# Kernel optimization log

Measured on AMD Instinct MI355X. Metric: run time of the kernel, lower is better.

## Reference

```python
import jax, jax.numpy as jnp
import numpy as np

EPS = 1e-5

def chan_layernorm(x, g):
    # LayerNorm over channel dim (-3), unbiased=False variance, learned scale g [C]
    mean = jnp.mean(x, axis=1, keepdims=True)
    var = jnp.var(x, axis=1, keepdims=True)
    return (x - mean) * jax.lax.rsqrt(var + EPS) * g[None, :, None, None]

def conv1x1(x, w):
    # w: [out_c, in_c]; pointwise conv == channel GEMM
    return jnp.einsum('bchw,oc->bohw', x, w)

def dwconv3x3(x, w):
    # depthwise 3x3, padding=1; w: [C, 1, 3, 3]
    C = x.shape[1]
    return jax.lax.conv_general_dilated(
        x, w, window_strides=(1, 1), padding='SAME',
        feature_group_count=C,
        dimension_numbers=('NCHW', 'OIHW', 'NCHW'))

def setup_inputs() -> dict:
    key = jax.random.key(0)
    ks = jax.random.split(key, 8)
    b, dim, x, y = 8, 512, 64, 64
    s1 = (dim ** -0.5) * 0.5  # modest init scale
    sd = (9 ** -0.5)
    return {
        'fmap': jax.random.normal(ks[0], (b, dim, x, y), jnp.float32),
        'g': jnp.ones((dim,), jnp.float32),
        'wq1': jax.random.normal(ks[1], (dim, dim), jnp.float32) * s1,
        'wq_dw': jax.random.normal(ks[2], (dim, 1, 3, 3), jnp.float32) * sd,
        'wk1': jax.random.normal(ks[3], (dim, dim), jnp.float32) * s1,
        'wk_dw': jax.random.normal(ks[4], (dim, 1, 3, 3), jnp.float32) * sd,
        'wv1': jax.random.normal(ks[5], (dim, dim), jnp.float32) * s1,
        'wv_dw': jax.random.normal(ks[6], (dim, 1, 3, 3), jnp.float32) * sd,
        'w_out': jax.random.normal(ks[7], (dim, dim), jnp.float32) * s1,
    }

def reference(fmap, g, wq1, wq_dw, wk1, wk_dw, wv1, wv_dw, w_out):
    b, dim, x, y = fmap.shape
    h = 8
    d = dim // h
    scale = d ** -0.5

    fm = chan_layernorm(fmap, g)
    q = dwconv3x3(conv1x1(fm, wq1), wq_dw)
    k = dwconv3x3(conv1x1(fm, wk1), wk_dw)
    v = dwconv3x3(conv1x1(fm, wv1), wv_dw)

    # b (h c) x y -> (b h) (x y) c
    def split_heads(t):
        return t.reshape(b, h, d, x * y).transpose(0, 1, 3, 2).reshape(b * h, x * y, d)
    q, k, v = map(split_heads, (q, k, v))

    q = jax.nn.softmax(q, axis=-1) * scale  # softmax over feature dim
    k = jax.nn.softmax(k, axis=-2)          # softmax over token dim

    ctx = jnp.einsum('bnd,bne->bde', k, v)  # [bh, d, d]
    out = jnp.einsum('bnd,bde->bne', q, ctx)  # [bh, n, d]

    # (b h) (x y) d -> b (h d) x y
    out = out.reshape(b, h, x * y, d).transpose(0, 1, 3, 2).reshape(b, h * d, x, y)
    out = jax.nn.silu(out)
    return conv1x1(out, w_out)
```

## Files before the change

### kernel.cpp

```cpp
#include <hip/hip_runtime.h>
#include <hip/hip_bf16.h>

typedef __attribute__((ext_vector_type(8))) short short8;
typedef __attribute__((ext_vector_type(4))) short shortx4;
typedef __attribute__((ext_vector_type(4))) float floatx4;

#define NB 8
#define C 512
#define NSP 4096
#define NHD 8
#define HDD 64

using bf16 = __hip_bfloat16;

__device__ __forceinline__ float b2f(bf16 v) { return __bfloat162float(v); }
__device__ __forceinline__ bf16 f2b(float f) { return __float2bfloat16(f); }
__device__ __forceinline__ float s2f(short s) {
    union { float f; unsigned u; } cv; cv.u = ((unsigned)(unsigned short)s) << 16; return cv.f;
}
__device__ __forceinline__ short f2s(float f) {
    bf16 b = f2b(f); return *reinterpret_cast<short*>(&b);
}

__device__ __forceinline__ void gl2lds16(const bf16* g, bf16* l) {
#if __has_builtin(__builtin_amdgcn_global_load_lds)
    __builtin_amdgcn_global_load_lds(
        (const __attribute__((address_space(1))) unsigned int*)g,
        (__attribute__((address_space(3))) unsigned int*)l, 16, 0, 0);
#else
    *(short8*)l = *(const short8*)g;
#endif
}

__global__ void detect_dtype(const unsigned* __restrict__ g_raw, int* __restrict__ flag) {
    *flag = (g_raw[0] == 0x3F800000u) ? 1 : 0;
}

__global__ __launch_bounds__(256) void prep_w(const void* g, const void* w1q, const void* wdq,
                                              const void* w1k, const void* wdk,
                                              const void* w1v, const void* wdv, const void* w1o,
                                              bf16* gc, bf16* wqkv, bf16* woutc,
                                              bf16* wkdc, bf16* wvdc, bf16* wqdT,
                                              const int* flag) {
    int i = blockIdx.x * 256 + threadIdx.x;
    int f = *flag;
    auto cv = [&](const void* s, int j) -> bf16 {
        return f ? f2b(((const float*)s)[j]) : ((const bf16*)s)[j];
    };
    if (i < C * C) {
        wqkv[i] = cv(w1q, i);
        wqkv[C * C + i] = cv(w1k, i);
        wqkv[2 * C * C + i] = cv(w1v, i);
        woutc[i] = cv(w1o, i);
    }
    if (i < C * 9) {
        int c = i / 9, t = i - c * 9;
        wqdT[t * C + c] = cv(wdq, i);
        wkdc[i] = cv(wdk, i);
        wvdc[i] = cv(wdv, i);
    }
    if (i < C) gc[i] = cv(g, i);
}

__global__ __launch_bounds__(256) void ln_fused(const void* __restrict__ fmap,
                                                const bf16* __restrict__ gc,
                                                bf16* __restrict__ fm,
                                                const int* __restrict__ flag) {
    const int P = 516;
    __shared__ bf16 T[32 * P];
    __shared__ float stat[32][2];
    int b = blockIdx.y;
    int n0 = blockIdx.x * 32;
    int t = threadIdx.x;
    if (*flag) {
        int nq = t & 7;
        int c0 = t >> 3;
        const float* src = (const float*)fmap + (size_t)b * C * NSP + n0 + nq * 4;
#pragma unroll 4
        for (int it = 0; it < 16; ++it) {
            int c = c0 + it * 32;
            float4 v = *(const float4*)(src + (size_t)c * NSP);
            T[(nq * 4 + 0) * P + c] = f2b(v.x);
            T[(nq * 4 + 1) * P + c] = f2b(v.y);
            T[(nq * 4 + 2) * P + c] = f2b(v.z);
            T[(nq * 4 + 3) * P + c] = f2b(v.w);
        }
    } else {
        int nq = t & 3;
        int c0 = t >> 2;
        const bf16* src = (const bf16*)fmap + (size_t)b * C * NSP + n0 + nq * 8;
#pragma unroll 4
        for (int it = 0; it < 8; ++it) {
            int c = c0 + it * 64;
            union { short8 s; short h[8]; } v;
            v.s = *(const short8*)(src + (size_t)c * NSP);
#pragma unroll
            for (int j = 0; j < 8; ++j)
                *(short*)&T[(nq * 8 + j) * P + c] = v.h[j];
        }
    }
    __syncthreads();
    int n = t >> 3, part = t & 7;
    {
        float s = 0.f, sq = 0.f;
        const bf16* row = T + n * P + part * 64;
#pragma unroll
        for (int i = 0; i < 8; ++i) {
            union { short8 v; short h[8]; } u;
            u.v = *(const short8*)(row + i * 8);
#pragma unroll
            for (int j = 0; j < 8; ++j) { float x = s2f(u.h[j]); s += x; sq += x * x; }
        }
#pragma unroll
        for (int off = 1; off < 8; off <<= 1) {
            s += __shfl_xor(s, off, 64);
            sq += __shfl_xor(sq, off, 64);
        }
        if (part == 0) {
            float mean = s * (1.f / C);
            float var = sq * (1.f / C) - mean * mean;
            stat[n][0] = mean;
            stat[n][1] = rsqrtf(var + 1e-5f);
        }
    }
    __syncthreads();
    float mean = stat[n][0], rs = stat[n][1];
    bf16* dst = fm + ((size_t)b * NSP + n0 + n) * C + part * 64;
    const bf16* row = T + n * P + part * 64;
    const bf16* gp = gc + part * 64;
#pragma unroll
    for (int i = 0; i < 8; ++i) {
        union { short8 v; short h[8]; } u, gv, ov;
        u.v = *(const short8*)(row + i * 8);
        gv.v = *(const short8*)(gp + i * 8);
#pragma unroll
        for (int j = 0; j < 8; ++j)
            ov.h[j] = f2s((s2f(u.h[j]) - mean) * rs * s2f(gv.h[j]));
        *(short8*)(dst + i * 8) = ov.v;
    }
}

template <int PHASE>
__global__ __launch_bounds__(512, 2) void gemm256(const bf16* __restrict__ X,
                                                  const bf16* __restrict__ Wall,
                                                  void* __restrict__ O0,
                                                  void* __restrict__ O1,
                                                  void* __restrict__ O2,
                                                  const int* __restrict__ flag) {
    __shared__ __align__(16) bf16 SH[4][256 * 64];
    bf16* SA0 = SH[0];
    bf16* SA1 = SH[1];
    bf16* SB0 = SH[2];
    bf16* SB1 = SH[3];
    const int nbase = blockIdx.x * 256;
    const int obase = blockIdx.y * 256;
    const int b = blockIdx.z;
    const int t = threadIdx.x;
    const int lane = t & 63, w = t >> 6;
    const int wm = w >> 2, wn = w & 3;
    const int m16 = lane & 15, q = lane >> 4;
    const bool AisW = (PHASE == 0) && (obase < 512);
    const bf16* gX = X + (size_t)b * NSP * C + (size_t)nbase * C;
    const bf16* gW = Wall + (size_t)obase * C;
    const bf16* gA = AisW ? gW : gX;
    const bf16* gB = AisW ? gX : gW;

    const int srow = t >> 3;
    const int sch = ((t & 7) ^ (srow & 7)) * 8;

    const int rA = wm * 128 + m16;
    const int rB = wn * 64 + m16;
    const int cs0 = ((q) ^ (m16 & 7)) * 8;
    const int cs1 = ((4 + q) ^ (m16 & 7)) * 8;

    floatx4 acc[8][4] = {};
    short8 Bf[4][2];

#define STAGE(LDS, G, K0, H)                                                   \
    {                                                                          \
        const bf16* _s = (G) + (size_t)((H) * 128 + srow) * C + (K0) + sch;    \
        bf16* _d = (LDS) + (H) * 8192 + t * 8;                                 \
        gl2lds16(_s, _d);                                                      \
        gl2lds16(_s + 64 * C, _d + 4096);                                      \
    }

#define VMW(N)                                                                 \
    {                                                                          \
        asm volatile("s_waitcnt vmcnt(" #N ")" ::: "memory");                  \
        __builtin_amdgcn_sched_barrier(0);                                     \
    }

#define PH(J, LA, LB, LOADB, STAGE_STMT, WAIT_STMT)                            \
    {                                                                          \
        short8 Af0, Af1, Af2, Af3;                                             \
        if (LOADB) {                                                           \
            _Pragma("unroll") for (int nt = 0; nt < 4; ++nt) {                 \
                Bf[nt][0] = *(const short8*)((LB) + (rB + nt * 16) * 64 + cs0);\
                Bf[nt][1] = *(const short8*)((LB) + (rB + nt * 16) * 64 + cs1);\
            }                                                                  \
        }                                                                      \
        Af0 = *(const short8*)((LA) + (rA + (2 * (J)) * 16) * 64 + cs0);       \
        Af1 = *(const short8*)((LA) + (rA + (2 * (J)) * 16) * 64 + cs1);       \
        Af2 = *(const short8*)((LA) + (rA + (2 * (J) + 1) * 16) * 64 + cs0);   \
        Af3 = *(const short8*)((LA) + (rA + (2 * (J) + 1) * 16) * 64 + cs1);   \
        STAGE_STMT;                                                            \
        WAIT_STMT;                                                             \
        __builtin_amdgcn_sched_barrier(0);                                     \
        __builtin_amdgcn_s_barrier();                                          \
        asm volatile("s_waitcnt lgkmcnt(0)" ::: "memory");                     \
        __builtin_amdgcn_sched_barrier(0);                                     \
        __builtin_amdgcn_s_setprio(1);                                         \
        _Pragma("unroll") for (int nt = 0; nt < 4; ++nt) {                     \
            acc[2 * (J)][nt] = __builtin_amdgcn_mfma_f32_16x16x32_bf16(        \
                Af0, Bf[nt][0], acc[2 * (J)][nt], 0, 0, 0);                    \
            acc[2 * (J)][nt] = __builtin_amdgcn_mfma_f32_16x16x32_bf16(        \
                Af1, Bf[nt][1], acc[2 * (J)][nt], 0, 0, 0);                    \
            acc[2 * (J) + 1][nt] = __builtin_amdgcn_mfma_f32_16x16x32_bf16(    \
                Af2, Bf[nt][0], acc[2 * (J) + 1][nt], 0, 0, 0);                \
            acc[2 * (J) + 1][nt] = __builtin_amdgcn_mfma_f32_16x16x32_bf16(    \
                Af3, Bf[nt][1], acc[2 * (J) + 1][nt], 0, 0, 0);                \
        }                                                                      \
        __builtin_amdgcn_s_setprio(0);                                         \
        __builtin_amdgcn_sched_barrier(0);                                     \
        __builtin_amdgcn_s_barrier();                                          \
    }

    STAGE(SA0, gA, 0, 0);
    STAGE(SA0, gA, 0, 1);
    STAGE(SB0, gB, 0, 0);
    STAGE(SB0, gB, 0, 1);
    STAGE(SB1, gB, 64, 0);
    STAGE(SB1, gB, 64, 1);
    VMW(0);
    __builtin_amdgcn_s_barrier();

    for (int i = 0; i < 3; ++i) {
        int kT = i * 128;
        PH(0, SA0, SB0, true,  STAGE(SA1, gA, kT + 64, 0),  ((void)0));
        PH(1, SA0, SB0, false, STAGE(SA1, gA, kT + 64, 1),  ((void)0));
        PH(2, SA0, SB0, false, STAGE(SB0, gB, kT + 128, 0), ((void)0));
        PH(3, SA0, SB0, false, STAGE(SB0, gB, kT + 128, 1), VMW(4));
        PH(0, SA1, SB1, true,  STAGE(SA0, gA, kT + 128, 0), ((void)0));
        PH(1, SA1, SB1, false, STAGE(SA0, gA, kT + 128, 1), ((void)0));
        PH(2, SA1, SB1, false, STAGE(SB1, gB, kT + 192, 0), ((void)0));
        PH(3, SA1, SB1, false, STAGE(SB1, gB, kT + 192, 1), VMW(4));
    }
    PH(0, SA0, SB0, true,  STAGE(SA1, gA, 448, 0), ((void)0));
    PH(1, SA0, SB0, false, STAGE(SA1, gA, 448, 1), ((void)0));
    PH(2, SA0, SB0, false, ((void)0), ((void)0));
    PH(3, SA0, SB0, false, ((void)0), VMW(0));
    PH(0, SA1, SB1, true,  ((void)0), ((void)0));
    PH(1, SA1, SB1, false, ((void)0), ((void)0));
    PH(2, SA1, SB1, false, ((void)0), ((void)0));
    PH(3, SA1, SB1, false, ((void)0), ((void)0));

#undef PH
#undef VMW
#undef STAGE

    if (PHASE == 0 && AisW) {
        bf16* out = (bf16*)O0 + (size_t)b * NSP * C;
#pragma unroll
        for (int nt = 0; nt < 4; ++nt)
#pragma unroll
            for (int mt = 0; mt < 8; ++mt) {
                int n = nbase + wn * 64 + nt * 16 + m16;
                int o = obase + wm * 128 + mt * 16 + q * 4;
                shortx4 pv;
#pragma unroll
                for (int r = 0; r < 4; ++r) pv[r] = f2s(acc[mt][nt][r]);
                *(shortx4*)(out + (size_t)n * C + o) = pv;
            }
    } else if (PHASE == 0) {
        bf16* out = (bf16*)((obase < 1024) ? O1 : O2) + (size_t)b * C * NSP;
        int ob = obase & 511;
#pragma unroll
        for (int nt = 0; nt < 4; ++nt)
#pragma unroll
            for (int mt = 0; mt < 8; ++mt) {
                int o = ob + wn * 64 + nt * 16 + m16;
                int n = nbase + wm * 128 + mt * 16 + q * 4;
                shortx4 pv;
#pragma unroll
                for (int r = 0; r < 4; ++r) pv[r] = f2s(acc[mt][nt][r]);
                *(shortx4*)(out + (size_t)o * NSP + n) = pv;
            }
    } else {
        int is_f32 = *flag;
        size_t outb = (size_t)b * C * NSP;
#pragma unroll
        for (int nt = 0; nt < 4; ++nt)
#pragma unroll
            for (int mt = 0; mt < 8; ++mt) {
                int o = obase + wn * 64 + nt * 16 + m16;
                int n = nbase + wm * 128 + mt * 16 + q * 4;
                size_t off = outb + (size_t)o * NSP + n;
                if (is_f32) {
                    *(floatx4*)((float*)O0 + off) = acc[mt][nt];
                } else {
                    shortx4 pv;
#pragma unroll
                    for (int r = 0; r < 4; ++r) pv[r] = f2s(acc[mt][nt][r]);
                    *(shortx4*)((bf16*)O0 + off) = pv;
                }
            }
    }
}

__global__ __launch_bounds__(256) void dwconv_nc8_sm(const bf16* __restrict__ X,
                                                     const bf16* __restrict__ WdT,
                                                     bf16* __restrict__ O) {
    int idx = blockIdx.x * 256 + threadIdx.x;
    int cg = idx & 63;
    int n = (idx >> 6) & (NSP - 1);
    int b = idx >> 18;
    int c0 = cg * 8;
    int y = n >> 6, x = n & 63;
    const bf16* xp = X + (size_t)b * NSP * C + c0;
    union { short8 s; short h[8]; } wv[9];
#pragma unroll
    for (int t = 0; t < 9; ++t) wv[t].s = *(const short8*)(WdT + t * C + c0);
    float acc[8] = {};
#pragma unroll
    for (int ky = 0; ky < 3; ++ky) {
        int yy = y + ky - 1;
        if ((unsigned)yy >= 64u) continue;
#pragma unroll
        for (int kx = 0; kx < 3; ++kx) {
            int xx = x + kx - 1;
            if ((unsigned)xx >= 64u) continue;
            union { short8 s; short h[8]; } iv;
            iv.s = *(const short8*)(xp + (size_t)(yy * 64 + xx) * C);
            int t = ky * 3 + kx;
#pragma unroll
            for (int i = 0; i < 8; ++i)
                acc[i] += s2f(iv.h[i]) * s2f(wv[t].h[i]);
        }
    }
    float mx = acc[0];
#pragma unroll
    for (int i = 1; i < 8; ++i) mx = fmaxf(mx, acc[i]);
#pragma unroll
    for (int off = 1; off < 8; off <<= 1) mx = fmaxf(mx, __shfl_xor(mx, off, 64));
    float e[8], s = 0.f;
#pragma unroll
    for (int i = 0; i < 8; ++i) { e[i] = __expf(acc[i] - mx); s += e[i]; }
#pragma unroll
    for (int off = 1; off < 8; off <<= 1) s += __shfl_xor(s, off, 64);
    float inv = 0.125f / s;
    union { short8 s; short h[8]; } ov;
#pragma unroll
    for (int i = 0; i < 8; ++i) ov.h[i] = f2s(e[i] * inv);
    *(short8*)(O + ((size_t)(b * NSP) + n) * C + c0) = ov.s;
}

__global__ __launch_bounds__(256) void dw_sk(const bf16* __restrict__ X,
                                             const bf16* __restrict__ Wd,
                                             bf16* __restrict__ O) {
    int bc = blockIdx.x;
    int c = bc & (C - 1);
    int t = threadIdx.x;
    int y = t >> 2, x0 = (t & 3) * 16;
    const bf16* xp = X + (size_t)bc * NSP;
    float wv[9];
#pragma unroll
    for (int i = 0; i < 9; ++i) wv[i] = b2f(Wd[c * 9 + i]);
    float a[16];
#pragma unroll
    for (int i = 0; i < 16; ++i) a[i] = 0.f;
#pragma unroll
    for (int ky = 0; ky < 3; ++ky) {
        int yy = y + ky - 1;
        if ((unsigned)yy >= 64u) continue;
        const bf16* rp = xp + yy * 64;
        float v[18];
        v[0] = (x0 > 0) ? b2f(rp[x0 - 1]) : 0.f;
        union { short8 s; short h[8]; } m0, m1;
        m0.s = *(const short8*)(rp + x0);
        m1.s = *(const short8*)(rp + x0 + 8);
#pragma unroll
        for (int j = 0; j < 8; ++j) { v[1 + j] = s2f(m0.h[j]); v[9 + j] = s2f(m1.h[j]); }
        v[17] = (x0 < 48) ? b2f(rp[x0 + 16]) : 0.f;
#pragma unroll
        for (int i = 0; i < 16; ++i)
            a[i] += wv[ky * 3 + 0] * v[i] + wv[ky * 3 + 1] * v[i + 1] + wv[ky * 3 + 2] * v[i + 2];
    }
    float mx = a[0];
#pragma unroll
    for (int i = 1; i < 16; ++i) mx = fmaxf(mx, a[i]);
#pragma unroll
    for (int off = 32; off; off >>= 1) mx = fmaxf(mx, __shfl_xor(mx, off, 64));
    __shared__ float red[4];
    __shared__ float bcv;
    int lane = t & 63, wid = t >> 6;
    if (lane == 0) red[wid] = mx;
    __syncthreads();
    if (t == 0) bcv = fmaxf(fmaxf(red[0], red[1]), fmaxf(red[2], red[3]));
    __syncthreads();
    float M = bcv;
    float s = 0.f;
#pragma unroll
    for (int i = 0; i < 16; ++i) { a[i] = __expf(a[i] - M); s += a[i]; }
#pragma unroll
    for (int off = 32; off; off >>= 1) s += __shfl_xor(s, off, 64);
    __syncthreads();
    if (lane == 0) red[wid] = s;
    __syncthreads();
    if (t == 0) bcv = red[0] + red[1] + red[2] + red[3];
    __syncthreads();
    float inv = 1.f / bcv;
    union { short8 s8; short h[8]; } o0, o1;
#pragma unroll
    for (int j = 0; j < 8; ++j) { o0.h[j] = f2s(a[j] * inv); o1.h[j] = f2s(a[8 + j] * inv); }
    bf16* op = O + (size_t)bc * NSP + y * 64 + x0;
    *(short8*)op = o0.s8;
    *(short8*)(op + 8) = o1.s8;
}

__global__ __launch_bounds__(256) void dwconv_cn8(const bf16* __restrict__ X,
                                                  const bf16* __restrict__ Wd,
                                                  bf16* __restrict__ O) {
    int idx = blockIdx.x * 256 + threadIdx.x;
    int g = idx & 511;
    int bc = idx >> 9;
    int c = bc & (C - 1);
    int y = g >> 3, x0 = (g & 7) * 8;
    const bf16* xp = X + (size_t)bc * NSP;
    float w[9];
#pragma unroll
    for (int t = 0; t < 9; ++t) w[t] = b2f(Wd[c * 9 + t]);
    float acc[8] = {};
#pragma unroll
    for (int ky = 0; ky < 3; ++ky) {
        int yy = y + ky - 1;
        if ((unsigned)yy >= 64u) continue;
        const bf16* rp = xp + yy * 64;
        union { short8 s; short h[8]; } mv;
        mv.s = *(const short8*)(rp + x0);
        float vals[10];
        vals[0] = (x0 > 0) ? b2f(rp[x0 - 1]) : 0.f;
#pragma unroll
        for (int i = 0; i < 8; ++i) vals[i + 1] = s2f(mv.h[i]);
        vals[9] = (x0 < 56) ? b2f(rp[x0 + 8]) : 0.f;
#pragma unroll
        for (int i = 0; i < 8; ++i)
            acc[i] += w[ky * 3 + 0] * vals[i] + w[ky * 3 + 1] * vals[i + 1] + w[ky * 3 + 2] * vals[i + 2];
    }
    union { short8 s; short h[8]; } ov;
#pragma unroll
    for (int i = 0; i < 8; ++i) ov.h[i] = f2s(acc[i]);
    *(short8*)(O + (size_t)bc * NSP + y * 64 + x0) = ov.s;
}

__global__ __launch_bounds__(256) void ctx_mfma(const bf16* __restrict__ K,
                                                const bf16* __restrict__ V,
                                                bf16* __restrict__ ctxb) {
    int bh = blockIdx.y;
    int b = bh >> 3, h = bh & 7;
    int lane = threadIdx.x & 63, w = threadIdx.x >> 6;
    int m16 = lane & 15, q = lane >> 4;
    int ebase = blockIdx.x * 16;
    const bf16* vp = V + ((size_t)b * C + h * 64 + ebase + m16) * NSP + q * 8;
    const bf16* kp = K + ((size_t)b * C + h * 64 + w * 16 + m16) * NSP + q * 8;
    floatx4 acc = {};
#pragma unroll 4
    for (int k0 = 0; k0 < NSP; k0 += 32) {
        short8 a = *(const short8*)(vp + k0);
        short8 bb = *(const short8*)(kp + k0);
        acc = __builtin_amdgcn_mfma_f32_16x16x32_bf16(a, bb, acc, 0, 0, 0);
    }
#pragma unroll
    for (int r = 0; r < 4; ++r) {
        int e = ebase + q * 4 + r;
        int d = w * 16 + m16;
        ctxb[((size_t)bh * 64 + e) * 64 + d] = f2b(acc[r]);
    }
}

__global__ __launch_bounds__(256) void attn_out(const bf16* __restrict__ Q,
                                                const bf16* __restrict__ ctxb,
                                                bf16* __restrict__ O) {
    int nbase = blockIdx.x * 64;
    int bh = blockIdx.y;
    int b = bh >> 3;
    int hb = (bh & 7) * 64;
    int lane = threadIdx.x & 63, w = threadIdx.x >> 6;
    int m16 = lane & 15, q = lane >> 4;
    const bf16* qp = Q + ((size_t)(b * NSP) + nbase + w * 16 + m16) * C + hb + q * 8;
    const bf16* cp = ctxb + ((size_t)bh * 64 + m16) * 64 + q * 8;
    floatx4 acc[4] = {};
#pragma unroll
    for (int ko = 0; ko < 64; ko += 32) {
        short8 a = *(const short8*)(qp + ko);
#pragma unroll
        for (int j = 0; j < 4; ++j) {
            short8 bf = *(const short8*)(cp + (size_t)j * 16 * 64 + ko);
            acc[j] = __builtin_amdgcn_mfma_f32_16x16x32_bf16(a, bf, acc[j], 0, 0, 0);
        }
    }
    bf16* op = O + (size_t)b * NSP * C;
#pragma unroll
    for (int j = 0; j < 4; ++j)
#pragma unroll
        for (int r = 0; r < 4; ++r) {
            int nrow = nbase + w * 16 + q * 4 + r;
            float x = acc[j][r];
            float sv = x / (1.f + __expf(-x));
            op[(size_t)nrow * C + hb + j * 16 + m16] = f2b(sv);
        }
}

extern "C" void kernel_launch(void* const* d_in, const int* in_sizes, int n_in,
                              void* d_out, int out_size, void* d_ws, size_t ws_size,
                              hipStream_t stream) {
    char* ws = (char*)d_ws;
    const size_t TB = (size_t)NB * NSP * C * 2;
    bf16* buf0 = (bf16*)(ws);
    bf16* buf1 = (bf16*)(ws + TB);
    bf16* buf2 = (bf16*)(ws + 2 * TB);
    bf16* buf3 = (bf16*)(ws + 3 * TB);
    char* ext = ws + 4 * TB;
    bf16* ctxb  = (bf16*)(ext);                   ext += 524288;
    bf16* gc    = (bf16*)(ext);                   ext += 4096;
    bf16* wqkv  = (bf16*)(ext);                   ext += 3 * C * C * 2;
    bf16* woutc = (bf16*)(ext);                   ext += C * C * 2;
    bf16* wkdc  = (bf16*)(ext);                   ext += 16384;
    bf16* wvdc  = (bf16*)(ext);                   ext += 16384;
    bf16* wqdT  = (bf16*)(ext);                   ext += 16384;
    int*  flag  = (int*)(ext);                    ext += 4096;

    detect_dtype<<<1, 1, 0, stream>>>((const unsigned*)d_in[1], flag);
    prep_w<<<(C * C + 255) / 256, 256, 0, stream>>>(d_in[1], d_in[2], d_in[3], d_in[4], d_in[5],
                                                    d_in[6], d_in[7], d_in[8],
                                                    gc, wqkv, woutc, wkdc, wvdc, wqdT, flag);

    ln_fused<<<dim3(NSP / 32, NB), 256, 0, stream>>>(d_in[0], gc, buf0, flag);

    gemm256<0><<<dim3(NSP / 256, 6, NB), 512, 0, stream>>>(buf0, wqkv, buf1, buf2, buf3, flag);

    dwconv_nc8_sm<<<NB * NSP * 64 / 256, 256, 0, stream>>>(buf1, wqdT, buf0);
    dw_sk<<<NB * C, 256, 0, stream>>>(buf2, wkdc, buf1);
    dwconv_cn8<<<NB * C * 512 / 256, 256, 0, stream>>>(buf3, wvdc, buf2);

    ctx_mfma<<<dim3(4, NB * NHD), 256, 0, stream>>>(buf1, buf2, ctxb);
    attn_out<<<dim3(NSP / 64, NB * NHD), 256, 0, stream>>>(buf0, ctxb, buf3);

    gemm256<1><<<dim3(NSP / 256, C / 256, NB), 512, 0, stream>>>(buf3, woutc, d_out, nullptr, nullptr, flag);
}
```

Before: 378.1 us.

## Fuse depthwise conv and softmax into the K/V context and Q attention kernels

Replaces five separate kernels (three depthwise convs with softmaxes, ctx GEMM, attn_out) with fused ones. kv_ctx computes the K/V depthwise convs on the fly over split row ranges and accumulates partial exp(K)ᵀV and normaliser sums via MFMA in LDS. A small kv_fin kernel reduces the partials and divides by the sums. q_attn fuses the Q depthwise conv, feature softmax, context product and SiLU. This removes several full-size intermediate tensor writes and reads. In exchange it skips the max subtraction in the K softmax, which risks overflow, and q_attn uses large LDS tiles that allow only low occupancy.

```diff
diff --git a/kernel.cpp b/kernel.cpp
--- a/kernel.cpp
+++ b/kernel.cpp
@@ -10,6 +10,7 @@
 #define NSP 4096
 #define NHD 8
 #define HDD 64
+#define KVPARTS 8
 
 using bf16 = __hip_bfloat16;
 
@@ -307,206 +308,221 @@
     }
 }
 
-__global__ __launch_bounds__(256) void dwconv_nc8_sm(const bf16* __restrict__ X,
-                                                     const bf16* __restrict__ WdT,
-                                                     bf16* __restrict__ O) {
-    int idx = blockIdx.x * 256 + threadIdx.x;
-    int cg = idx & 63;
-    int n = (idx >> 6) & (NSP - 1);
-    int b = idx >> 18;
-    int c0 = cg * 8;
-    int y = n >> 6, x = n & 63;
-    const bf16* xp = X + (size_t)b * NSP * C + c0;
-    union { short8 s; short h[8]; } wv[9];
-#pragma unroll
-    for (int t = 0; t < 9; ++t) wv[t].s = *(const short8*)(WdT + t * C + c0);
-    float acc[8] = {};
-#pragma unroll
-    for (int ky = 0; ky < 3; ++ky) {
-        int yy = y + ky - 1;
-        if ((unsigned)yy >= 64u) continue;
-#pragma unroll
-        for (int kx = 0; kx < 3; ++kx) {
-            int xx = x + kx - 1;
-            if ((unsigned)xx >= 64u) continue;
-            union { short8 s; short h[8]; } iv;
-            iv.s = *(const short8*)(xp + (size_t)(yy * 64 + xx) * C);
-            int t = ky * 3 + kx;
-#pragma unroll
-            for (int i = 0; i < 8; ++i)
-                acc[i] += s2f(iv.h[i]) * s2f(wv[t].h[i]);
-        }
-    }
-    float mx = acc[0];
-#pragma unroll
-    for (int i = 1; i < 8; ++i) mx = fmaxf(mx, acc[i]);
-#pragma unroll
-    for (int off = 1; off < 8; off <<= 1) mx = fmaxf(mx, __shfl_xor(mx, off, 64));
-    float e[8], s = 0.f;
-#pragma unroll
-    for (int i = 0; i < 8; ++i) { e[i] = __expf(acc[i] - mx); s += e[i]; }
-#pragma unroll
-    for (int off = 1; off < 8; off <<= 1) s += __shfl_xor(s, off, 64);
-    float inv = 0.125f / s;
-    union { short8 s; short h[8]; } ov;
-#pragma unroll
-    for (int i = 0; i < 8; ++i) ov.h[i] = f2s(e[i] * inv);
-    *(short8*)(O + ((size_t)(b * NSP) + n) * C + c0) = ov.s;
-}
-
-__global__ __launch_bounds__(256) void dw_sk(const bf16* __restrict__ X,
-                                             const bf16* __restrict__ Wd,
-                                             bf16* __restrict__ O) {
-    int bc = blockIdx.x;
-    int c = bc & (C - 1);
+__device__ __forceinline__ void load_row10(float* v, const bf16* rp0, int yy, int x0) {
+    if ((unsigned)yy >= 64u) {
+#pragma unroll
+        for (int j = 0; j < 10; ++j) v[j] = 0.f;
+        return;
+    }
+    const bf16* rp = rp0 + yy * 64;
+    v[0] = (x0 > 0) ? b2f(rp[x0 - 1]) : 0.f;
+    union { short8 s; short h[8]; } m;
+    m.s = *(const short8*)(rp + x0);
+#pragma unroll
+    for (int j = 0; j < 8; ++j) v[1 + j] = s2f(m.h[j]);
+    v[9] = (x0 < 56) ? b2f(rp[x0 + 8]) : 0.f;
+}
+
+__global__ __launch_bounds__(512) void kv_ctx(const bf16* __restrict__ Kpre,
+                                              const bf16* __restrict__ Vpre,
+                                              const bf16* __restrict__ wkd,
+                                              const bf16* __restrict__ wvd,
+                                              float* __restrict__ Apart,
+                                              float* __restrict__ Zpart) {
+    __shared__ __align__(16) bf16 KB[2][64 * 64];
+    __shared__ __align__(16) bf16 VB[2][64 * 64];
+    const int part = blockIdx.x;
+    const int bh = blockIdx.y;
+    const int b = bh >> 3, h = bh & 7;
+    const int t = threadIdx.x;
+    const int ch = t >> 3;
+    const int xo = t & 7, x0 = xo * 8;
+    const int c = h * 64 + ch;
+    const bf16* kp = Kpre + ((size_t)b * C + c) * NSP;
+    const bf16* vp = Vpre + ((size_t)b * C + c) * NSP;
+    float wk[9], wv[9];
+#pragma unroll
+    for (int i = 0; i < 9; ++i) { wk[i] = b2f(wkd[c * 9 + i]); wv[i] = b2f(wvd[c * 9 + i]); }
+    const int ybase = part * (64 / KVPARTS);
+    float k3[3][10], v3[3][10];
+    load_row10(k3[0], kp, ybase - 1, x0);
+    load_row10(k3[1], kp, ybase, x0);
+    load_row10(v3[0], vp, ybase - 1, x0);
+    load_row10(v3[1], vp, ybase, x0);
+    float zsum = 0.f;
+    const int lane = t & 63, w = t >> 6;
+    const int et = w >> 1, wd = w & 1;
+    const int m16 = lane & 15, q = lane >> 4;
+    const int arow = et * 16 + m16;
+    const int br0 = wd * 32 + m16;
+    floatx4 acc[2] = {};
+    for (int yy = 0; yy < 64 / KVPARTS; ++yy) {
+        const int buf = yy & 1;
+        load_row10(k3[2], kp, ybase + yy + 1, x0);
+        load_row10(v3[2], vp, ybase + yy + 1, x0);
+        float ak[8] = {}, av[8] = {};
+#pragma unroll
+        for (int ky = 0; ky < 3; ++ky)
+#pragma unroll
+            for (int i = 0; i < 8; ++i) {
+                ak[i] += wk[ky * 3 + 0] * k3[ky][i] + wk[ky * 3 + 1] * k3[ky][i + 1] + wk[ky * 3 + 2] * k3[ky][i + 2];
+                av[i] += wv[ky * 3 + 0] * v3[ky][i] + wv[ky * 3 + 1] * v3[ky][i + 1] + wv[ky * 3 + 2] * v3[ky][i + 2];
+            }
+        union { short8 s; short h[8]; } ke, ve;
+#pragma unroll
+        for (int i = 0; i < 8; ++i) {
+            float e = __expf(ak[i]);
+            zsum += e;
+            ke.h[i] = f2s(e);
+            ve.h[i] = f2s(av[i]);
+        }
+        const int chunk = xo ^ (ch & 7);
+        *(short8*)(&KB[buf][ch * 64 + chunk * 8]) = ke.s;
+        *(short8*)(&VB[buf][ch * 64 + chunk * 8]) = ve.s;
+#pragma unroll
+        for (int j = 0; j < 10; ++j) {
+            k3[0][j] = k3[1][j]; k3[1][j] = k3[2][j];
+            v3[0][j] = v3[1][j]; v3[1][j] = v3[2][j];
+        }
+        __syncthreads();
+#pragma unroll
+        for (int kh = 0; kh < 2; ++kh) {
+            short8 Af = *(const short8*)(&VB[buf][arow * 64 + (((kh * 4 + q) ^ (arow & 7)) * 8)]);
+#pragma unroll
+            for (int dt = 0; dt < 2; ++dt) {
+                int brow = br0 + dt * 16;
+                short8 Bfm = *(const short8*)(&KB[buf][brow * 64 + (((kh * 4 + q) ^ (brow & 7)) * 8)]);
+                acc[dt] = __builtin_amdgcn_mfma_f32_16x16x32_bf16(Af, Bfm, acc[dt], 0, 0, 0);
+            }
+        }
+    }
+#pragma unroll
+    for (int off = 1; off < 8; off <<= 1) zsum += __shfl_xor(zsum, off, 64);
+    if ((lane & 7) == 0)
+        Zpart[((size_t)bh * KVPARTS + part) * 64 + ch] = zsum;
+#pragma unroll
+    for (int dt = 0; dt < 2; ++dt)
+#pragma unroll
+        for (int r = 0; r < 4; ++r) {
+            int e = et * 16 + q * 4 + r;
+            int d = wd * 32 + dt * 16 + m16;
+            Apart[(((size_t)bh * KVPARTS + part) * 64 + e) * 64 + d] = acc[dt][r];
+        }
+}
+
+__global__ __launch_bounds__(256) void kv_fin(const float* __restrict__ Apart,
+                                              const float* __restrict__ Zpart,
+                                              bf16* __restrict__ ctxb) {
+    int bh = blockIdx.x;
     int t = threadIdx.x;
-    int y = t >> 2, x0 = (t & 3) * 16;
-    const bf16* xp = X + (size_t)bc * NSP;
-    float wv[9];
-#pragma unroll
-    for (int i = 0; i < 9; ++i) wv[i] = b2f(Wd[c * 9 + i]);
-    float a[16];
-#pragma unroll
-    for (int i = 0; i < 16; ++i) a[i] = 0.f;
-#pragma unroll
-    for (int ky = 0; ky < 3; ++ky) {
-        int yy = y + ky - 1;
-        if ((unsigned)yy >= 64u) continue;
-        const bf16* rp = xp + yy * 64;
-        float v[18];
-        v[0] = (x0 > 0) ? b2f(rp[x0 - 1]) : 0.f;
-        union { short8 s; short h[8]; } m0, m1;
-        m0.s = *(const short8*)(rp + x0);
-        m1.s = *(const short8*)(rp + x0 + 8);
-#pragma unroll
-        for (int j = 0; j < 8; ++j) { v[1 + j] = s2f(m0.h[j]); v[9 + j] = s2f(m1.h[j]); }
-        v[17] = (x0 < 48) ? b2f(rp[x0 + 16]) : 0.f;
-#pragma unroll
-        for (int i = 0; i < 16; ++i)
-            a[i] += wv[ky * 3 + 0] * v[i] + wv[ky * 3 + 1] * v[i + 1] + wv[ky * 3 + 2] * v[i + 2];
-    }
-    float mx = a[0];
-#pragma unroll
-    for (int i = 1; i < 16; ++i) mx = fmaxf(mx, a[i]);
-#pragma unroll
-    for (int off = 32; off; off >>= 1) mx = fmaxf(mx, __shfl_xor(mx, off, 64));
-    __shared__ float red[4];
-    __shared__ float bcv;
-    int lane = t & 63, wid = t >> 6;
-    if (lane == 0) red[wid] = mx;
+    int e = t >> 2, dq = (t & 3) * 16;
+    float z[16] = {}, a[16] = {};
+#pragma unroll
+    for (int p = 0; p < KVPARTS; ++p) {
+        const float* zp = Zpart + ((size_t)bh * KVPARTS + p) * 64 + dq;
+        const float* ap = Apart + (((size_t)bh * KVPARTS + p) * 64 + e) * 64 + dq;
+#pragma unroll
+        for (int j = 0; j < 16; ++j) { z[j] += zp[j]; a[j] += ap[j]; }
+    }
+    bf16* op = ctxb + ((size_t)bh * 64 + e) * 64 + dq;
+#pragma unroll
+    for (int j = 0; j < 16; ++j) op[j] = f2b(a[j] / z[j]);
+}
+
+__global__ __launch_bounds__(256) void q_attn(const bf16* __restrict__ Qpre,
+                                              const bf16* __restrict__ WdT,
+                                              const bf16* __restrict__ ctxb,
+                                              bf16* __restrict__ O) {
+    __shared__ __align__(16) bf16 P[64 * 512];
+    __shared__ __align__(16) bf16 CT[8 * 64 * 64];
+    const int y = blockIdx.x, b = blockIdx.y;
+    const int t = threadIdx.x;
+#pragma unroll
+    for (int j = 0; j < 16; ++j) {
+        int idx = t + j * 256;
+        int h = idx >> 9, e = (idx >> 3) & 63, co = idx & 7;
+        short8 vv = *(const short8*)(ctxb + (((size_t)(b * 8 + h) * 64 + e) * 64 + co * 8));
+        *(short8*)(&CT[h * 4096 + e * 64 + ((co ^ (e & 7)) * 8)]) = vv;
+    }
+    const int lane = t & 63, wvw = t >> 6;
+    const int co = lane;
+    const bf16* qp = Qpre + (size_t)b * NSP * C + co * 8;
+    union sh8 { short8 s; short h[8]; };
+    sh8 w9[9];
+#pragma unroll
+    for (int tap = 0; tap < 9; ++tap) w9[tap].s = *(const short8*)(WdT + tap * C + co * 8);
+    sh8 cw[3][3];
+    const int x0 = wvw * 16;
+    auto ldc = [&](int ny, int nx) -> short8 {
+        if ((unsigned)ny >= 64u || (unsigned)nx >= 64u) { short8 z = {}; return z; }
+        return *(const short8*)(qp + (size_t)(ny * 64 + nx) * C);
+    };
+#pragma unroll
+    for (int dy = 0; dy < 3; ++dy) {
+        cw[dy][0].s = ldc(y + dy - 1, x0 - 1);
+        cw[dy][1].s = ldc(y + dy - 1, x0);
+    }
+#pragma unroll 2
+    for (int xi = 0; xi < 16; ++xi) {
+        const int x = x0 + xi;
+#pragma unroll
+        for (int dy = 0; dy < 3; ++dy) cw[dy][2].s = ldc(y + dy - 1, x + 1);
+        float a8[8] = {};
+#pragma unroll
+        for (int dy = 0; dy < 3; ++dy)
+#pragma unroll
+            for (int dc = 0; dc < 3; ++dc)
+#pragma unroll
+                for (int i = 0; i < 8; ++i)
+                    a8[i] += s2f(w9[dy * 3 + dc].h[i]) * s2f(cw[dy][dc].h[i]);
+        float mx = a8[0];
+#pragma unroll
+        for (int i = 1; i < 8; ++i) mx = fmaxf(mx, a8[i]);
+#pragma unroll
+        for (int off = 1; off < 8; off <<= 1) mx = fmaxf(mx, __shfl_xor(mx, off, 64));
+        float e8[8], s = 0.f;
+#pragma unroll
+        for (int i = 0; i < 8; ++i) { e8[i] = __expf(a8[i] - mx); s += e8[i]; }
+#pragma unroll
+        for (int off = 1; off < 8; off <<= 1) s += __shfl_xor(s, off, 64);
+        float inv = 0.125f / s;
+        union sh8 pv;
+#pragma unroll
+        for (int i = 0; i < 8; ++i) pv.h[i] = f2s(e8[i] * inv);
+        *(short8*)(&P[x * 512 + ((co ^ (x & 7)) * 8)]) = pv.s;
+#pragma unroll
+        for (int dy = 0; dy < 3; ++dy) { cw[dy][0] = cw[dy][1]; cw[dy][1] = cw[dy][2]; }
+    }
     __syncthreads();
-    if (t == 0) bcv = fmaxf(fmaxf(red[0], red[1]), fmaxf(red[2], red[3]));
-    __syncthreads();
-    float M = bcv;
-    float s = 0.f;
-#pragma unroll
-    for (int i = 0; i < 16; ++i) { a[i] = __expf(a[i] - M); s += a[i]; }
-#pragma unroll
-    for (int off = 32; off; off >>= 1) s += __shfl_xor(s, off, 64);
-    __syncthreads();
-    if (lane == 0) red[wid] = s;
-    __syncthreads();
-    if (t == 0) bcv = red[0] + red[1] + red[2] + red[3];
-    __syncthreads();
-    float inv = 1.f / bcv;
-    union { short8 s8; short h[8]; } o0, o1;
-#pragma unroll
-    for (int j = 0; j < 8; ++j) { o0.h[j] = f2s(a[j] * inv); o1.h[j] = f2s(a[8 + j] * inv); }
-    bf16* op = O + (size_t)bc * NSP + y * 64 + x0;
-    *(short8*)op = o0.s8;
-    *(short8*)(op + 8) = o1.s8;
-}
-
-__global__ __launch_bounds__(256) void dwconv_cn8(const bf16* __restrict__ X,
-                                                  const bf16* __restrict__ Wd,
-                                                  bf16* __restrict__ O) {
-    int idx = blockIdx.x * 256 + threadIdx.x;
-    int g = idx & 511;
-    int bc = idx >> 9;
-    int c = bc & (C - 1);
-    int y = g >> 3, x0 = (g & 7) * 8;
-    const bf16* xp = X + (size_t)bc * NSP;
-    float w[9];
-#pragma unroll
-    for (int t = 0; t < 9; ++t) w[t] = b2f(Wd[c * 9 + t]);
-    float acc[8] = {};
-#pragma unroll
-    for (int ky = 0; ky < 3; ++ky) {
-        int yy = y + ky - 1;
-        if ((unsigned)yy >= 64u) continue;
-        const bf16* rp = xp + yy * 64;
-        union { short8 s; short h[8]; } mv;
-        mv.s = *(const short8*)(rp + x0);
-        float vals[10];
-        vals[0] = (x0 > 0) ? b2f(rp[x0 - 1]) : 0.f;
-#pragma unroll
-        for (int i = 0; i < 8; ++i) vals[i + 1] = s2f(mv.h[i]);
-        vals[9] = (x0 < 56) ? b2f(rp[x0 + 8]) : 0.f;
-#pragma unroll
-        for (int i = 0; i < 8; ++i)
-            acc[i] += w[ky * 3 + 0] * vals[i] + w[ky * 3 + 1] * vals[i + 1] + w[ky * 3 + 2] * vals[i + 2];
-    }
-    union { short8 s; short h[8]; } ov;
-#pragma unroll
-    for (int i = 0; i < 8; ++i) ov.h[i] = f2s(acc[i]);
-    *(short8*)(O + (size_t)bc * NSP + y * 64 + x0) = ov.s;
-}
-
-__global__ __launch_bounds__(256) void ctx_mfma(const bf16* __restrict__ K,
-                                                const bf16* __restrict__ V,
-                                                bf16* __restrict__ ctxb) {
-    int bh = blockIdx.y;
-    int b = bh >> 3, h = bh & 7;
-    int lane = threadIdx.x & 63, w = threadIdx.x >> 6;
-    int m16 = lane & 15, q = lane >> 4;
-    int ebase = blockIdx.x * 16;
-    const bf16* vp = V + ((size_t)b * C + h * 64 + ebase + m16) * NSP + q * 8;
-    const bf16* kp = K + ((size_t)b * C + h * 64 + w * 16 + m16) * NSP + q * 8;
-    floatx4 acc = {};
-#pragma unroll 4
-    for (int k0 = 0; k0 < NSP; k0 += 32) {
-        short8 a = *(const short8*)(vp + k0);
-        short8 bb = *(const short8*)(kp + k0);
-        acc = __builtin_amdgcn_mfma_f32_16x16x32_bf16(a, bb, acc, 0, 0, 0);
-    }
-#pragma unroll
-    for (int r = 0; r < 4; ++r) {
-        int e = ebase + q * 4 + r;
-        int d = w * 16 + m16;
-        ctxb[((size_t)bh * 64 + e) * 64 + d] = f2b(acc[r]);
-    }
-}
-
-__global__ __launch_bounds__(256) void attn_out(const bf16* __restrict__ Q,
-                                                const bf16* __restrict__ ctxb,
-                                                bf16* __restrict__ O) {
-    int nbase = blockIdx.x * 64;
-    int bh = blockIdx.y;
-    int b = bh >> 3;
-    int hb = (bh & 7) * 64;
-    int lane = threadIdx.x & 63, w = threadIdx.x >> 6;
-    int m16 = lane & 15, q = lane >> 4;
-    const bf16* qp = Q + ((size_t)(b * NSP) + nbase + w * 16 + m16) * C + hb + q * 8;
-    const bf16* cp = ctxb + ((size_t)bh * 64 + m16) * 64 + q * 8;
-    floatx4 acc[4] = {};
-#pragma unroll
-    for (int ko = 0; ko < 64; ko += 32) {
-        short8 a = *(const short8*)(qp + ko);
-#pragma unroll
-        for (int j = 0; j < 4; ++j) {
-            short8 bf = *(const short8*)(cp + (size_t)j * 16 * 64 + ko);
-            acc[j] = __builtin_amdgcn_mfma_f32_16x16x32_bf16(a, bf, acc[j], 0, 0, 0);
-        }
-    }
-    bf16* op = O + (size_t)b * NSP * C;
-#pragma unroll
-    for (int j = 0; j < 4; ++j)
-#pragma unroll
-        for (int r = 0; r < 4; ++r) {
-            int nrow = nbase + w * 16 + q * 4 + r;
-            float x = acc[j][r];
-            float sv = x / (1.f + __expf(-x));
-            op[(size_t)nrow * C + hb + j * 16 + m16] = f2b(sv);
+    const int m16 = lane & 15, q = lane >> 4;
+    const int nrow = wvw * 16 + m16;
+    floatx4 acc[8][4] = {};
+#pragma unroll
+    for (int kh = 0; kh < 2; ++kh) {
+#pragma unroll
+        for (int h2 = 0; h2 < 8; ++h2) {
+            int lc = h2 * 8 + kh * 4 + q;
+            short8 Bfr = *(const short8*)(&P[nrow * 512 + ((lc ^ (nrow & 7)) * 8)]);
+#pragma unroll
+            for (int et = 0; et < 4; ++et) {
+                int erow = et * 16 + m16;
+                short8 Afr = *(const short8*)(&CT[h2 * 4096 + erow * 64 + (((kh * 4 + q) ^ (erow & 7)) * 8)]);
+                acc[h2][et] = __builtin_amdgcn_mfma_f32_16x16x32_bf16(Afr, Bfr, acc[h2][et], 0, 0, 0);
+            }
+        }
+    }
+    bf16* op = O + ((size_t)b * NSP + (size_t)y * 64 + wvw * 16 + m16) * C;
+#pragma unroll
+    for (int h2 = 0; h2 < 8; ++h2)
+#pragma unroll
+        for (int et = 0; et < 4; ++et) {
+            shortx4 pv;
+#pragma unroll
+            for (int r = 0; r < 4; ++r) {
+                float xv = acc[h2][et][r];
+                pv[r] = f2s(xv / (1.f + __expf(-xv)));
+            }
+            *(shortx4*)(op + h2 * 64 + et * 16 + q * 4) = pv;
         }
 }
 
@@ -528,6 +544,8 @@
     bf16* wvdc  = (bf16*)(ext);                   ext += 16384;
     bf16* wqdT  = (bf16*)(ext);                   ext += 16384;
     int*  flag  = (int*)(ext);                    ext += 4096;
+    float* Apart = (float*)buf0;
+    float* Zpart = Apart + (size_t)NB * NHD * KVPARTS * 64 * 64;
 
     detect_dtype<<<1, 1, 0, stream>>>((const unsigned*)d_in[1], flag);
     prep_w<<<(C * C + 255) / 256, 256, 0, stream>>>(d_in[1], d_in[2], d_in[3], d_in[4], d_in[5],
@@ -538,12 +556,10 @@
 
     gemm256<0><<<dim3(NSP / 256, 6, NB), 512, 0, stream>>>(buf0, wqkv, buf1, buf2, buf3, flag);
 
-    dwconv_nc8_sm<<<NB * NSP * 64 / 256, 256, 0, stream>>>(buf1, wqdT, buf0);
-    dw_sk<<<NB * C, 256, 0, stream>>>(buf2, wkdc, buf1);
-    dwconv_cn8<<<NB * C * 512 / 256, 256, 0, stream>>>(buf3, wvdc, buf2);
-
-    ctx_mfma<<<dim3(4, NB * NHD), 256, 0, stream>>>(buf1, buf2, ctxb);
-    attn_out<<<dim3(NSP / 64, NB * NHD), 256, 0, stream>>>(buf0, ctxb, buf3);
-
-    gemm256<1><<<dim3(NSP / 256, C / 256, NB), 512, 0, stream>>>(buf3, woutc, d_out, nullptr, nullptr, flag);
-}
+    kv_ctx<<<dim3(KVPARTS, NB * NHD), 512, 0, stream>>>(buf2, buf3, wkdc, wvdc, Apart, Zpart);
+    kv_fin<<<NB * NHD, 256, 0, stream>>>(Apart, Zpart, ctxb);
+
+    q_attn<<<dim3(64, NB), 256, 0, stream>>>(buf1, wqdT, ctxb, buf2);
+
+    gemm256<1><<<dim3(NSP / 256, C / 256, NB), 512, 0, stream>>>(buf2, woutc, d_out, nullptr, nullptr, flag);
+}
```

Result: faster. 340.9 us (-9.8%).
